# Performance work log

Measured on AMD Instinct MI355X. Metric: run time of the kernel, lower is better.

The kernel has to match this reference:

```python
import jax, jax.numpy as jnp
import numpy as np

# Dims from init_kwargs / input_specs
C_IN, H, W = 128, 224, 224
C_OUT, KH, KW = 256, 3, 3
STRIDE = 1  # padding='valid'


def setup_inputs() -> dict:
    key = jax.random.key(0)
    k1, k2 = jax.random.split(key)
    x = jax.random.normal(k1, (C_IN, H, W), dtype=jnp.float32)
    kernels = jax.random.normal(k2, (C_OUT, C_IN, KH, KW), dtype=jnp.float32) * 0.05
    return {"x": x, "kernels": kernels}


def reference(x, kernels):
    # Original does im2col + matmul, which is exactly a valid cross-correlation
    # (no kernel flip). Express it as a direct conv: (1,C,H,W) * (O,I,kh,kw).
    out = jax.lax.conv_general_dilated(
        x[None],                      # (1, C_in, H, W)
        kernels,                      # (C_out, C_in, KH, KW)
        window_strides=(STRIDE, STRIDE),
        padding="VALID",
        dimension_numbers=("NCHW", "OIHW", "NCHW"),
    )
    return out[0]                     # (C_out, H_out, W_out) = (256, 222, 222)
```

## Files before the change

kernel.cpp:

```cpp
#include <hip/hip_runtime.h>

#define CIN   128
#define HH    224
#define WW    224
#define COUT  256
#define HO    222
#define WO    222
#define HWSZ  (224 * 224)
#define PLANE (224 * 224 * 64)

typedef unsigned short u16;
typedef unsigned int   u32;
typedef __bf16  bf16x8 __attribute__((ext_vector_type(8)));
typedef float   f32x4  __attribute__((ext_vector_type(4)));

__device__ __forceinline__ u16 f2bf(float f) {
  union { float f; u32 u; } v; v.f = f;
  u32 u = v.u;
  return (u16)((u + 0x7FFFu + ((u >> 16) & 1u)) >> 16);
}

__global__ __launch_bounds__(256) void prep(const float* __restrict__ x,
                                            const float* __restrict__ w,
                                            u16* __restrict__ xp,
                                            u16* __restrict__ wp) {
  const int t = threadIdx.x;
  if (blockIdx.x < 784) {
#pragma unroll
    for (int i = 0; i < 4; ++i) {
      int U   = (blockIdx.x * 4 + i) * 256 + t;
      int g   = U & 7;
      int U2  = U >> 3;
      int ww  = U2 % 224;
      int t2  = U2 / 224;
      int h   = t2 % 224;
      int ch  = t2 / 224;
      const float* src = x + (size_t)(ch * 64 + ((g ^ (ww & 7)) * 8)) * HWSZ +
                         h * WW + ww;
      u16 o[8];
#pragma unroll
      for (int e = 0; e < 8; ++e)
        o[e] = f2bf(src[(size_t)e * HWSZ]);
      uint4 v;
      v.x = (u32)o[0] | ((u32)o[1] << 16);
      v.y = (u32)o[2] | ((u32)o[3] << 16);
      v.z = (u32)o[4] | ((u32)o[5] << 16);
      v.w = (u32)o[6] | ((u32)o[7] << 16);
      *(uint4*)(&xp[(size_t)ch * PLANE + (size_t)(h * WW + ww) * 64 + g * 8]) = v;
    }
  } else {
    int u    = (blockIdx.x - 784) * 256 + t;
    int jcp  = u & 7;
    int mr   = (u >> 3) & 127;
    int rest = u >> 10;
    int kw   = rest % 3;
    int q    = rest / 3;
    int ch   = q & 1;
    int r    = q >> 1;
    int kh   = r % 3;
    int mt   = r / 3;
    int oc   = mt * 128 + mr;
    int cb   = ch * 64 + (jcp ^ (mr & 7)) * 8;
    u16 o[8];
#pragma unroll
    for (int e = 0; e < 8; ++e)
      o[e] = f2bf(w[((size_t)(oc * CIN + cb + e) * 3 + kh) * 3 + kw]);
    uint4 v;
    v.x = (u32)o[0] | ((u32)o[1] << 16);
    v.y = (u32)o[2] | ((u32)o[3] << 16);
    v.z = (u32)o[4] | ((u32)o[5] << 16);
    v.w = (u32)o[6] | ((u32)o[7] << 16);
    *(uint4*)(&wp[(size_t)u * 8]) = v;
  }
}

__device__ __forceinline__ void lds_dma16(const u16* g, u16* l) {
  __builtin_amdgcn_global_load_lds(
      reinterpret_cast<__attribute__((address_space(1))) u32*>(
          reinterpret_cast<uintptr_t>(g)),
      reinterpret_cast<__attribute__((address_space(3))) u32*>(
          reinterpret_cast<uintptr_t>(l)),
      16, 0, 0);
}

__global__ __launch_bounds__(256, 4) void conv_mfma(const u16* __restrict__ wp,
                                                    const u16* __restrict__ xp,
                                                    float* __restrict__ out) {
  __shared__ u16 ldsB[2][8192];

  const int tid  = threadIdx.x;
  const int lane = tid & 63;
  const int wave = tid >> 6;
  const int quad = lane >> 4;
  const int lr   = lane & 15;

  const int bx  = blockIdx.x;
  const int xcd = bx & 7;
  const int u   = xcd * 111 + (bx >> 3);
  const int oh  = u >> 2;
  const int mt  = (u >> 1) & 1;
  const int nt  = u & 1;

  f32x4 acc[2][7];
#pragma unroll
  for (int i = 0; i < 2; ++i)
#pragma unroll
    for (int j = 0; j < 7; ++j) acc[i][j] = {0.f, 0.f, 0.f, 0.f};

  int swA[2];
#pragma unroll
  for (int ks = 0; ks < 2; ++ks)
    swA[ks] = ((ks * 4 + quad) ^ (lr & 7)) << 3;

  {
    const u16* g0 = xp + (size_t)oh * (WW * 64) + nt * (112 * 64);
#pragma unroll
    for (int uu = 0; uu < 4; ++uu) {
      const int unit = wave * 4 + uu;
      lds_dma16(g0 + unit * 512 + lane * 8, &ldsB[0][unit * 512]);
    }
  }
  __syncthreads();

#pragma unroll 1
  for (int s = 0; s < 6; ++s) {
    const int cur = s & 1;

    if (s < 5) {
      const int sn  = s + 1;
      const u16* gn = xp + (size_t)(sn & 1) * PLANE +
                      (size_t)(oh + (sn >> 1)) * (WW * 64) + nt * (112 * 64);
      u16* dst = &ldsB[cur ^ 1][0];
#pragma unroll
      for (int uu = 0; uu < 4; ++uu) {
        const int unit = wave * 4 + uu;
        lds_dma16(gn + unit * 512 + lane * 8, dst + unit * 512);
      }
    }

    const int ch = s & 1;
    const int kh = s >> 1;

    const u16* Ab = wp + (size_t)((mt * 3 + kh) * 2 + ch) * 24576 +
                    wave * 2048 + lr * 64;
    const u16* Bb = &ldsB[cur][0];

#pragma unroll
    for (int kw = 0; kw < 3; ++kw) {
      const int bq  = (lr + kw) * 64;
      const int sw7 = (lr + kw) & 7;
#pragma unroll
      for (int ks = 0; ks < 2; ++ks) {
        const int swB = ((ks * 4 + quad) ^ sw7) << 3;
        bf16x8 af[2], bg[7];
#pragma unroll
        for (int i = 0; i < 2; ++i)
          af[i] = *reinterpret_cast<const bf16x8*>(Ab + kw * 8192 + i * 1024 + swA[ks]);
#pragma unroll
        for (int j = 0; j < 7; ++j)
          bg[j] = *reinterpret_cast<const bf16x8*>(Bb + bq + j * 1024 + swB);
#pragma unroll
        for (int i = 0; i < 2; ++i)
#pragma unroll
          for (int j = 0; j < 7; ++j)
            acc[i][j] = __builtin_amdgcn_mfma_f32_16x16x32_bf16(af[i], bg[j], acc[i][j], 0, 0, 0);
      }
    }

    __syncthreads();
  }

  const int mb = mt * 128 + wave * 32;
#pragma unroll
  for (int i = 0; i < 2; ++i) {
#pragma unroll
    for (int j = 0; j < 7; ++j) {
      const int col = nt * 112 + j * 16 + lr;
      if (col < WO) {
        float* op = out + (size_t)(mb + i * 16 + quad * 4) * (HO * WO) +
                    (size_t)oh * WO + col;
#pragma unroll
        for (int r = 0; r < 4; ++r)
          op[(size_t)r * (HO * WO)] = acc[i][j][r];
      }
    }
  }
}

__global__ void conv_naive(const float* __restrict__ x, const float* __restrict__ w,
                           float* __restrict__ out) {
  int idx = blockIdx.x * 256 + threadIdx.x;
  if (idx >= COUT * HO * WO) return;
  int ow  = idx % WO;
  int tmp = idx / WO;
  int oh  = tmp % HO;
  int oc  = tmp / HO;
  float s = 0.f;
  for (int c = 0; c < CIN; ++c)
    for (int kh = 0; kh < 3; ++kh) {
      const float* xr = &x[(size_t)(c * HH + oh + kh) * WW + ow];
      const float* wr = &w[((size_t)(oc * CIN + c) * 3 + kh) * 3];
      s += xr[0] * wr[0] + xr[1] * wr[1] + xr[2] * wr[2];
    }
  out[idx] = s;
}

extern "C" void kernel_launch(void* const* d_in, const int* in_sizes, int n_in,
                              void* d_out, int out_size, void* d_ws, size_t ws_size,
                              hipStream_t stream) {
  const float* x    = (const float*)d_in[0];
  const float* kern = (const float*)d_in[1];
  float* out        = (float*)d_out;

  const size_t WP_BYTES = (size_t)36864 * 16;
  const size_t XP_BYTES = (size_t)2 * PLANE * 2;

  if (ws_size >= WP_BYTES + XP_BYTES) {
    u16* wp = (u16*)d_ws;
    u16* xp = (u16*)((char*)d_ws + WP_BYTES);
    hipLaunchKernelGGL(prep, dim3(928), dim3(256), 0, stream, x, kern, xp, wp);
    hipLaunchKernelGGL(conv_mfma, dim3(888), dim3(256), 0, stream, wp, xp, out);
  } else {
    int total = COUT * HO * WO;
    hipLaunchKernelGGL(conv_naive, dim3((total + 255) / 256), dim3(256), 0, stream,
                       x, kern, out);
  }
}
```

Baseline: 123.3 us.

## Fuse input bf16 conversion into conv kernel with register-staged prefetch

Removes the separate pass that converted and relaid out the whole input tensor to bf16 in workspace. The conv kernel now loads fp32 input rows directly into registers, converts and swizzles them into LDS, and prefetches two stages ahead through registers instead of using direct global-to-LDS DMA. This saves a full read and write of the input but adds register pressure, so the occupancy hint drops from 4 to 2 blocks, and each input row is now converted redundantly by the several blocks that read it.

```diff
diff --git a/kernel.cpp b/kernel.cpp
--- a/kernel.cpp
+++ b/kernel.cpp
@@ -7,7 +7,6 @@
 #define HO    222
 #define WO    222
 #define HWSZ  (224 * 224)
-#define PLANE (224 * 224 * 64)
 
 typedef unsigned short u16;
 typedef unsigned int   u32;
@@ -20,71 +19,33 @@
   return (u16)((u + 0x7FFFu + ((u >> 16) & 1u)) >> 16);
 }
 
-__global__ __launch_bounds__(256) void prep(const float* __restrict__ x,
-                                            const float* __restrict__ w,
-                                            u16* __restrict__ xp,
-                                            u16* __restrict__ wp) {
-  const int t = threadIdx.x;
-  if (blockIdx.x < 784) {
-#pragma unroll
-    for (int i = 0; i < 4; ++i) {
-      int U   = (blockIdx.x * 4 + i) * 256 + t;
-      int g   = U & 7;
-      int U2  = U >> 3;
-      int ww  = U2 % 224;
-      int t2  = U2 / 224;
-      int h   = t2 % 224;
-      int ch  = t2 / 224;
-      const float* src = x + (size_t)(ch * 64 + ((g ^ (ww & 7)) * 8)) * HWSZ +
-                         h * WW + ww;
-      u16 o[8];
-#pragma unroll
-      for (int e = 0; e < 8; ++e)
-        o[e] = f2bf(src[(size_t)e * HWSZ]);
-      uint4 v;
-      v.x = (u32)o[0] | ((u32)o[1] << 16);
-      v.y = (u32)o[2] | ((u32)o[3] << 16);
-      v.z = (u32)o[4] | ((u32)o[5] << 16);
-      v.w = (u32)o[6] | ((u32)o[7] << 16);
-      *(uint4*)(&xp[(size_t)ch * PLANE + (size_t)(h * WW + ww) * 64 + g * 8]) = v;
-    }
-  } else {
-    int u    = (blockIdx.x - 784) * 256 + t;
-    int jcp  = u & 7;
-    int mr   = (u >> 3) & 127;
-    int rest = u >> 10;
-    int kw   = rest % 3;
-    int q    = rest / 3;
-    int ch   = q & 1;
-    int r    = q >> 1;
-    int kh   = r % 3;
-    int mt   = r / 3;
-    int oc   = mt * 128 + mr;
-    int cb   = ch * 64 + (jcp ^ (mr & 7)) * 8;
-    u16 o[8];
-#pragma unroll
-    for (int e = 0; e < 8; ++e)
-      o[e] = f2bf(w[((size_t)(oc * CIN + cb + e) * 3 + kh) * 3 + kw]);
-    uint4 v;
-    v.x = (u32)o[0] | ((u32)o[1] << 16);
-    v.y = (u32)o[2] | ((u32)o[3] << 16);
-    v.z = (u32)o[4] | ((u32)o[5] << 16);
-    v.w = (u32)o[6] | ((u32)o[7] << 16);
-    *(uint4*)(&wp[(size_t)u * 8]) = v;
-  }
-}
-
-__device__ __forceinline__ void lds_dma16(const u16* g, u16* l) {
-  __builtin_amdgcn_global_load_lds(
-      reinterpret_cast<__attribute__((address_space(1))) u32*>(
-          reinterpret_cast<uintptr_t>(g)),
-      reinterpret_cast<__attribute__((address_space(3))) u32*>(
-          reinterpret_cast<uintptr_t>(l)),
-      16, 0, 0);
-}
-
-__global__ __launch_bounds__(256, 4) void conv_mfma(const u16* __restrict__ wp,
-                                                    const u16* __restrict__ xp,
+__global__ void prep_w(const float* __restrict__ w, u16* __restrict__ wp) {
+  int u    = blockIdx.x * 256 + threadIdx.x;
+  int jcp  = u & 7;
+  int mr   = (u >> 3) & 127;
+  int rest = u >> 10;
+  int kw   = rest % 3;
+  int q    = rest / 3;
+  int ch   = q & 1;
+  int r    = q >> 1;
+  int kh   = r % 3;
+  int mt   = r / 3;
+  int oc   = mt * 128 + mr;
+  int cb   = ch * 64 + (jcp ^ (mr & 7)) * 8;
+  u16 o[8];
+#pragma unroll
+  for (int e = 0; e < 8; ++e)
+    o[e] = f2bf(w[((size_t)(oc * CIN + cb + e) * 3 + kh) * 3 + kw]);
+  uint4 v;
+  v.x = (u32)o[0] | ((u32)o[1] << 16);
+  v.y = (u32)o[2] | ((u32)o[3] << 16);
+  v.z = (u32)o[4] | ((u32)o[5] << 16);
+  v.w = (u32)o[6] | ((u32)o[7] << 16);
+  *(uint4*)(&wp[(size_t)u * 8]) = v;
+}
+
+__global__ __launch_bounds__(256, 2) void conv_mfma(const u16* __restrict__ wp,
+                                                    const float* __restrict__ x,
                                                     float* __restrict__ out) {
   __shared__ u16 ldsB[2][8192];
 
@@ -93,6 +54,8 @@
   const int wave = tid >> 6;
   const int quad = lane >> 4;
   const int lr   = lane & 15;
+  const int cl   = tid & 127;
+  const int ghi  = tid >> 7;
 
   const int bx  = blockIdx.x;
   const int xcd = bx & 7;
@@ -101,6 +64,9 @@
   const int mt  = (u >> 1) & 1;
   const int nt  = u & 1;
 
+  int colg = nt * 112 + cl;
+  if (colg > 223) colg = 223;
+
   f32x4 acc[2][7];
 #pragma unroll
   for (int i = 0; i < 2; ++i)
@@ -112,34 +78,43 @@
   for (int ks = 0; ks < 2; ++ks)
     swA[ks] = ((ks * 4 + quad) ^ (lr & 7)) << 3;
 
-  {
-    const u16* g0 = xp + (size_t)oh * (WW * 64) + nt * (112 * 64);
-#pragma unroll
-    for (int uu = 0; uu < 4; ++uu) {
-      const int unit = wave * 4 + uu;
-      lds_dma16(g0 + unit * 512 + lane * 8, &ldsB[0][unit * 512]);
-    }
-  }
+  float xs[4][8];
+
+  auto STAGE_LOAD = [&](int s) {
+    const int row = oh + (s >> 1);
+    const float* base = x + (size_t)((s & 1) * 64) * HWSZ + (size_t)row * WW + colg;
+#pragma unroll
+    for (int it = 0; it < 4; ++it) {
+      const float* src = base + (size_t)((it * 2 + ghi) * 8) * HWSZ;
+#pragma unroll
+      for (int e = 0; e < 8; ++e)
+        xs[it][e] = src[(size_t)e * HWSZ];
+    }
+  };
+  auto STAGE_WRITE = [&](u16* buf) {
+#pragma unroll
+    for (int it = 0; it < 4; ++it) {
+      const int g  = it * 2 + ghi;
+      const int jc = g ^ (cl & 7);
+      uint4 v;
+      v.x = (u32)f2bf(xs[it][0]) | ((u32)f2bf(xs[it][1]) << 16);
+      v.y = (u32)f2bf(xs[it][2]) | ((u32)f2bf(xs[it][3]) << 16);
+      v.z = (u32)f2bf(xs[it][4]) | ((u32)f2bf(xs[it][5]) << 16);
+      v.w = (u32)f2bf(xs[it][6]) | ((u32)f2bf(xs[it][7]) << 16);
+      *(uint4*)(&buf[cl * 64 + jc * 8]) = v;
+    }
+  };
+
+  STAGE_LOAD(0);
+  STAGE_WRITE(&ldsB[0][0]);
   __syncthreads();
+  STAGE_LOAD(1);
 
 #pragma unroll 1
   for (int s = 0; s < 6; ++s) {
     const int cur = s & 1;
-
-    if (s < 5) {
-      const int sn  = s + 1;
-      const u16* gn = xp + (size_t)(sn & 1) * PLANE +
-                      (size_t)(oh + (sn >> 1)) * (WW * 64) + nt * (112 * 64);
-      u16* dst = &ldsB[cur ^ 1][0];
-#pragma unroll
-      for (int uu = 0; uu < 4; ++uu) {
-        const int unit = wave * 4 + uu;
-        lds_dma16(gn + unit * 512 + lane * 8, dst + unit * 512);
-      }
-    }
-
-    const int ch = s & 1;
-    const int kh = s >> 1;
+    const int ch  = s & 1;
+    const int kh  = s >> 1;
 
     const u16* Ab = wp + (size_t)((mt * 3 + kh) * 2 + ch) * 24576 +
                     wave * 2048 + lr * 64;
@@ -167,6 +142,10 @@
       }
     }
 
+    if (s < 5) {
+      STAGE_WRITE(&ldsB[cur ^ 1][0]);
+      if (s < 4) STAGE_LOAD(s + 2);
+    }
     __syncthreads();
   }
 
@@ -213,13 +192,11 @@
   float* out        = (float*)d_out;
 
   const size_t WP_BYTES = (size_t)36864 * 16;
-  const size_t XP_BYTES = (size_t)2 * PLANE * 2;
-
-  if (ws_size >= WP_BYTES + XP_BYTES) {
+
+  if (ws_size >= WP_BYTES) {
     u16* wp = (u16*)d_ws;
-    u16* xp = (u16*)((char*)d_ws + WP_BYTES);
-    hipLaunchKernelGGL(prep, dim3(928), dim3(256), 0, stream, x, kern, xp, wp);
-    hipLaunchKernelGGL(conv_mfma, dim3(888), dim3(256), 0, stream, wp, xp, out);
+    hipLaunchKernelGGL(prep_w, dim3(144), dim3(256), 0, stream, kern, wp);
+    hipLaunchKernelGGL(conv_mfma, dim3(888), dim3(256), 0, stream, wp, x, out);
   } else {
     int total = COUT * HO * WO;
     hipLaunchKernelGGL(conv_naive, dim3((total + 255) / 256), dim3(256), 0, stream,
```

New measurement: 120.6 us. 1.02x faster.
